# Optimization experiments

Hardware: AMD Instinct MI355X
Metric: run time of the kernel (lower is better)

## Reference

```python
import jax, jax.numpy as jnp
import numpy as np

B, D, H, Z, E = 2048, 1024, 1024, 256, 64


def setup_inputs() -> dict:
    key = jax.random.key(0)
    ks = jax.random.split(key, 16)
    s = lambda k, shape, std=0.02: jax.random.normal(k, shape, dtype=jnp.float32) * std
    return {
        "x": jax.random.normal(ks[0], (B, D), dtype=jnp.float32),
        "h0": jax.random.normal(ks[1], (B, H), dtype=jnp.float32),
        "c0": jax.random.normal(ks[2], (B, H), dtype=jnp.float32),
        "hhat0": jax.random.normal(ks[3], (B, Z), dtype=jnp.float32),
        "chat0": jax.random.normal(ks[4], (B, Z), dtype=jnp.float32),
        "hweight": s(ks[5], (Z + H + D, 4 * Z)),
        "hbias": jnp.zeros((4 * Z,), jnp.float32),
        "zweight_h": s(ks[6], (Z, 4 * E), 0.01),
        "zweight_x": s(ks[7], (Z, 4 * E), 0.01),
        "zweight_b": s(ks[8], (Z, 4 * E), 0.01),
        "zbias_h": jnp.ones((4 * E,), jnp.float32),
        "zbias_x": jnp.ones((4 * E,), jnp.float32),
        # stacked in gate order (i, g, f, o), matching the torch cat order
        "dweight_h": jnp.full((4, E, H), 0.1 / E, jnp.float32),
        "dweight_x": jnp.full((4, E, H), 0.1 / E, jnp.float32),
        "dweight_b": s(ks[9], (4, E, H), 0.01),
        "weight": s(ks[10], (H + D, 4 * H)),
        "bias": jnp.zeros((4 * H,), jnp.float32),
    }


def reference(x, h0, c0, hhat0, chat0, hweight, hbias,
              zweight_h, zweight_x, zweight_b, zbias_h, zbias_x,
              dweight_h, dweight_x, dweight_b, weight, bias):
    # ---- hyper LSTM cell ----
    hcat = jnp.concatenate([hhat0, h0, x], axis=1)                 # [B, Z+H+D]
    hg = hcat @ hweight + hbias                                    # [B, 4Z]
    i_h, g_h, f_h, o_h = jnp.split(hg, 4, axis=1)
    chat1 = jax.nn.sigmoid(f_h) * chat0 + jax.nn.sigmoid(i_h) * jnp.tanh(g_h)
    hhat1 = jax.nn.sigmoid(o_h) * jnp.tanh(chat1)                  # [B, Z]

    # ---- embeddings z (gate order i, g, f, o) ----
    z_h = (hhat1 @ zweight_h + zbias_h).reshape(-1, 4, E)          # [B,4,E]
    z_x = (hhat1 @ zweight_x + zbias_x).reshape(-1, 4, E)
    z_b = (hhat1 @ zweight_b).reshape(-1, 4, E)

    # ---- per-gate modulation vectors d_y* : [B,4,H] -> [B,4H] ----
    d_yh = jnp.einsum('bge,geh->bgh', z_h, dweight_h).reshape(-1, 4 * H)
    d_yx = jnp.einsum('bge,geh->bgh', z_x, dweight_x).reshape(-1, 4 * H)
    d_yb = jnp.einsum('bge,geh->bgh', z_b, dweight_b).reshape(-1, 4 * H)

    # ---- main LSTM with hypernetwork modulation ----
    gates = jnp.concatenate([h0, x], axis=1) @ weight              # [B, 4H]
    gates = gates * d_yh * d_yx + d_yb + bias
    i_g, g_g, f_g, o_g = jnp.split(gates, 4, axis=1)
    c1 = jax.nn.sigmoid(f_g) * c0 + jax.nn.sigmoid(i_g) * jnp.tanh(g_g)
    h1 = jax.nn.sigmoid(o_g) * jnp.tanh(c1)
    return (h1, c1, hhat1, chat1)
```

## Files before the change

### kernel.cpp

```cpp
#include <hip/hip_runtime.h>
#include <hip/hip_bf16.h>
#include <math.h>


typedef __attribute__((ext_vector_type(8))) short bf16x8;
typedef __attribute__((ext_vector_type(4))) float f32x4;
typedef unsigned short u16;

__device__ __forceinline__ u16 f2b(float f) {
  union { float f; unsigned u; } v; v.f = f;
  unsigned r = v.u + 0x7fffu + ((v.u >> 16) & 1u);
  return (u16)(r >> 16);
}
__device__ __forceinline__ float b2f(u16 b) {
  union { unsigned u; float f; } v; v.u = ((unsigned)b) << 16; return v.f;
}
__device__ __forceinline__ float sigm(float x) {
  return __builtin_amdgcn_rcpf(1.f + __expf(-x));
}
__device__ __forceinline__ float ftanh(float x) {
  float xc = fminf(fmaxf(x, -15.f), 15.f);
  float t = __expf(2.f * xc);
  return (t - 1.f) * __builtin_amdgcn_rcpf(t + 1.f);
}
__device__ __forceinline__ float sel4(float a, float b, float c, float d, int k) {
  return (k & 2) ? ((k & 1) ? d : c) : ((k & 1) ? b : a);
}

#define GLL16(gsrc, ldst)                                                      \
  __builtin_amdgcn_global_load_lds(                                            \
      (const __attribute__((address_space(1))) void*)(gsrc),                   \
      (__attribute__((address_space(3))) void*)(ldst), 16, 0, 0)

__global__ void k_prep(const float* __restrict__ hhat0, const float* __restrict__ h0,
                       const float* __restrict__ x, const float* __restrict__ weight,
                       const float* __restrict__ hweight,
                       const float* __restrict__ zw_h, const float* __restrict__ zw_x,
                       const float* __restrict__ zw_b, const float* __restrict__ dw_h,
                       const float* __restrict__ dw_x, const float* __restrict__ dw_b,
                       u16* __restrict__ hcatb, u16* __restrict__ bt,
                       u16* __restrict__ zwT, u16* __restrict__ dwT) {
  __shared__ float tile[32][66];
  int bid = blockIdx.x;
  const int t = threadIdx.x;
  if (bid < 4608) {
    int i = bid * 256 + t;
    int b = i / 576, c4 = i % 576;
    const float* src;
    if (c4 < 64)       src = hhat0 + (long)b * 256 + c4 * 4;
    else if (c4 < 320) src = h0 + (long)b * 1024 + (c4 - 64) * 4;
    else               src = x + (long)b * 1024 + (c4 - 320) * 4;
    float4 v = *(const float4*)src;
    ushort4 o = {f2b(v.x), f2b(v.y), f2b(v.z), f2b(v.w)};
    *(ushort4*)&hcatb[(long)b * 2304 + c4 * 4] = o;
    return;
  }
  bid -= 4608;
  if (bid < 5760) {
    const int n0 = (bid % 160) * 32, k0 = (bid / 160) * 64;
    if (n0 < 4096 && k0 < 256) return;
    const int isH = (n0 >= 4096);
    const float* src; int C, sc0, sr0;
    if (isH) { src = hweight; C = 1024; sc0 = n0 - 4096; sr0 = k0; }
    else     { src = weight;  C = 4096; sc0 = n0;        sr0 = k0 - 256; }
    #pragma unroll
    for (int p = 0; p < 8; ++p) {
      int c = t & 31, r = (t >> 5) + 8 * p;
      tile[c][r] = src[(long)(sr0 + r) * C + sc0 + c];
    }
    __syncthreads();
    #pragma unroll
    for (int p = 0; p < 2; ++p) {
      int kc = t & 15, cl = (t >> 4) + 16 * p;
      int orow;
      if (isH) { int u = sc0 + cl; orow = 4096 + ((u & 255) << 2) + (u >> 8); }
      else     orow = n0 + cl;
      ushort4 o = {f2b(tile[cl][4 * kc]), f2b(tile[cl][4 * kc + 1]),
                   f2b(tile[cl][4 * kc + 2]), f2b(tile[cl][4 * kc + 3])};
      *(ushort4*)&bt[(long)orow * 2304 + k0 + 4 * kc] = o;
    }
    return;
  }
  bid -= 5760;
  const int zi = bid >> 5, bx = bid & 31;
  const float* src; u16* dst; int R, C;
  if (zi < 3) {
    src = (zi == 0) ? zw_h : (zi == 1) ? zw_x : zw_b;
    dst = zwT + (long)zi * 65536; R = 256; C = 256;
  } else {
    int s = zi - 3, tt = s >> 2, g = s & 3;
    src = ((tt == 0) ? dw_h : (tt == 1) ? dw_x : dw_b) + (long)g * 65536;
    dst = dwT + (long)s * 65536; R = 64; C = 1024;
  }
  const int nct = C / 32;
  const int c0 = (bx % nct) * 32, r0 = (bx / nct) * 64;
  #pragma unroll
  for (int p = 0; p < 8; ++p) {
    int c = t & 31, r = (t >> 5) + 8 * p;
    tile[c][r] = src[(long)(r0 + r) * C + c0 + c];
  }
  __syncthreads();
  #pragma unroll
  for (int p = 0; p < 2; ++p) {
    int kc = t & 15, cl = (t >> 4) + 16 * p;
    ushort4 o = {f2b(tile[cl][4 * kc]), f2b(tile[cl][4 * kc + 1]),
                 f2b(tile[cl][4 * kc + 2]), f2b(tile[cl][4 * kc + 3])};
    *(ushort4*)&dst[(long)(c0 + cl) * R + r0 + 4 * kc] = o;
  }
}

__global__ __launch_bounds__(512, 4)
void k_gemm_main(const u16* __restrict__ A, const u16* __restrict__ Bt,
                 const float* __restrict__ hbias, const float* __restrict__ chat0,
                 u16* __restrict__ grawb, float* __restrict__ chat1,
                 float* __restrict__ hhat1, u16* __restrict__ hhat1b) {
  constexpr int K = 2304, BK = 64;
  __shared__ __align__(16) u16 sA[128 * BK];
  __shared__ __align__(16) u16 sB[128 * BK];
  const int m0 = blockIdx.y * 128, n0 = blockIdx.x * 128;
  const int kstart = (n0 < 4096) ? 256 : 0;
  const int tid = threadIdx.x, wave = tid >> 6, lane = tid & 63;
  const int quad = lane >> 4, lrow = lane & 15;
  const int wm = (wave >> 2) * 64, wn = (wave & 3) * 32;

  const int la = tid * 16;
  const int rowa = la >> 7, qa = (((la >> 4) & 7) - rowa) & 7;
  const int lb = 8192 + tid * 16;
  const int rowb = lb >> 7, qb = (((lb >> 4) & 7) - rowb) & 7;
  const long aoff0 = ((long)(m0 + rowa) * K + qa * 8) * 2;
  const long aoff1 = ((long)(m0 + rowb) * K + qb * 8) * 2;
  const long boff0 = ((long)(n0 + rowa) * K + qa * 8) * 2;
  const long boff1 = ((long)(n0 + rowb) * K + qb * 8) * 2;

  const f32x4 vz = {0.f, 0.f, 0.f, 0.f};
  f32x4 acc[4][2];
  #pragma unroll
  for (int i = 0; i < 4; ++i)
    #pragma unroll
    for (int j = 0; j < 2; ++j) acc[i][j] = vz;

  for (int k0 = kstart; k0 < K; k0 += BK) {
    GLL16((const char*)A + aoff0 + (long)k0 * 2, (char*)sA + wave * 1024);
    GLL16((const char*)A + aoff1 + (long)k0 * 2, (char*)sA + 8192 + wave * 1024);
    GLL16((const char*)Bt + boff0 + (long)k0 * 2, (char*)sB + wave * 1024);
    GLL16((const char*)Bt + boff1 + (long)k0 * 2, (char*)sB + 8192 + wave * 1024);
    __syncthreads();

    bf16x8 af[4][2], bf[2][2];
    #pragma unroll
    for (int i = 0; i < 4; ++i) {
      int row = wm + i * 16 + lrow;
      const char* base = (const char*)sA + row * 128;
      af[i][0] = *(const bf16x8*)(base + (((quad + row) & 7) << 4));
      af[i][1] = *(const bf16x8*)(base + (((4 + quad + row) & 7) << 4));
    }
    #pragma unroll
    for (int j = 0; j < 2; ++j) {
      int row = wn + j * 16 + lrow;
      const char* base = (const char*)sB + row * 128;
      bf[j][0] = *(const bf16x8*)(base + (((quad + row) & 7) << 4));
      bf[j][1] = *(const bf16x8*)(base + (((4 + quad + row) & 7) << 4));
    }
    #pragma unroll
    for (int kk = 0; kk < 2; ++kk)
      #pragma unroll
      for (int i = 0; i < 4; ++i)
        #pragma unroll
        for (int j = 0; j < 2; ++j)
          acc[i][j] = __builtin_amdgcn_mfma_f32_16x16x32_bf16(af[i][kk], bf[j][kk], acc[i][j], 0, 0, 0);
    __syncthreads();
  }

  if (n0 < 4096) {
    #pragma unroll
    for (int i = 0; i < 4; ++i)
      #pragma unroll
      for (int j = 0; j < 2; ++j)
        #pragma unroll
        for (int r = 0; r < 4; ++r) {
          int row = m0 + wm + i * 16 + quad * 4 + r;
          int col = n0 + wn + j * 16 + lrow;
          grawb[(long)row * 4096 + col] = f2b(acc[i][j][r]);
        }
  } else {
    const int ubase = (n0 - 4096) + wn;
    const int q3 = lane & 3;
    #pragma unroll
    for (int i = 0; i < 4; ++i) {
      #pragma unroll
      for (int j = 0; j < 2; ++j) {
        int u = ubase + j * 16 + lrow;
        int g = u & 3, z = u >> 2;
        float hb = hbias[g * 256 + z];
        float v0 = acc[i][j][0] + hb, v1 = acc[i][j][1] + hb;
        float v2 = acc[i][j][2] + hb, v3 = acc[i][j][3] + hb;
        float s0 = sel4(v0, v1, v2, v3, q3);
        float s1 = __shfl_xor(sel4(v0, v1, v2, v3, q3 ^ 1), 1);
        float s2 = __shfl_xor(sel4(v0, v1, v2, v3, q3 ^ 2), 2);
        float s3 = __shfl_xor(sel4(v0, v1, v2, v3, q3 ^ 3), 3);
        float vi = sel4(s0, s1, s2, s3, q3);
        float vg = sel4(s0, s1, s2, s3, q3 ^ 1);
        float vf = sel4(s0, s1, s2, s3, q3 ^ 2);
        float vo = sel4(s0, s1, s2, s3, q3 ^ 3);
        int row = m0 + wm + i * 16 + quad * 4 + q3;
        float cc = sigm(vf) * chat0[(long)row * 256 + z] + sigm(vi) * ftanh(vg);
        float hh = sigm(vo) * ftanh(cc);
        chat1[(long)row * 256 + z] = cc;
        hhat1[(long)row * 256 + z] = hh;
        hhat1b[(long)row * 256 + z] = f2b(hh);
      }
    }
  }
}

__global__ __launch_bounds__(256, 2)
void k_gemm_z(const u16* __restrict__ A, const u16* __restrict__ Bt,
              const float* __restrict__ zbh, const float* __restrict__ zbx,
              u16* __restrict__ zbout) {
  constexpr int K = 256, BK = 32;
  __shared__ __align__(16) u16 sA[64 * BK];
  __shared__ __align__(16) u16 sB[128 * BK];
  const int m0 = blockIdx.y * 64, n0 = blockIdx.x * 128;
  const int tid = threadIdx.x, wave = tid >> 6, lane = tid & 63;
  const int quad = lane >> 4, lrow = lane & 15;
  const int wm = (wave >> 1) * 32, wn = (wave & 1) * 64;

  const int sl = tid * 16;
  const int arow = sl >> 6;
  const int aq = (((sl & 63) >> 4) - (arow >> 1)) & 3;
  const long aoff = ((long)(m0 + arow) * K) * 2 + aq * 16;

  const f32x4 vz = {0.f, 0.f, 0.f, 0.f};
  f32x4 acc[2][4];
  #pragma unroll
  for (int i = 0; i < 2; ++i)
    #pragma unroll
    for (int j = 0; j < 4; ++j) acc[i][j] = vz;

  for (int k0 = 0; k0 < K; k0 += BK) {
    GLL16((const char*)A + aoff + (long)k0 * 2, (char*)sA + wave * 1024);
    #pragma unroll
    for (int c = 0; c < 2; ++c) {
      int l = c * 4096 + sl;
      int row = l >> 6;
      int q = (((l & 63) >> 4) - (row >> 1)) & 3;
      const char* g = (const char*)Bt + ((long)(n0 + row) * K + k0) * 2 + q * 16;
      GLL16(g, (char*)sB + c * 4096 + wave * 1024);
    }
    __syncthreads();
    bf16x8 af[2], bf[4];
    #pragma unroll
    for (int i = 0; i < 2; ++i) {
      int row = wm + i * 16 + lrow;
      af[i] = *(const bf16x8*)((const char*)sA + row * 64 + (((quad + (row >> 1)) & 3) << 4));
    }
    #pragma unroll
    for (int j = 0; j < 4; ++j) {
      int row = wn + j * 16 + lrow;
      bf[j] = *(const bf16x8*)((const char*)sB + row * 64 + (((quad + (row >> 1)) & 3) << 4));
    }
    #pragma unroll
    for (int i = 0; i < 2; ++i)
      #pragma unroll
      for (int j = 0; j < 4; ++j)
        acc[i][j] = __builtin_amdgcn_mfma_f32_16x16x32_bf16(af[i], bf[j], acc[i][j], 0, 0, 0);
    __syncthreads();
  }
  #pragma unroll
  for (int i = 0; i < 2; ++i) {
    #pragma unroll
    for (int j = 0; j < 4; ++j) {
      #pragma unroll
      for (int r = 0; r < 4; ++r) {
        int row = m0 + wm + i * 16 + quad * 4 + r;
        int col = n0 + wn + j * 16 + lrow;
        float v = acc[i][j][r] + ((col < 256) ? zbh[col] : (col < 512) ? zbx[col - 256] : 0.f);
        zbout[(long)row * 768 + col] = f2b(v);
      }
    }
  }
}

__global__ __launch_bounds__(256, 2)
void k_dmod_lstm(const u16* __restrict__ z, const u16* __restrict__ dwT,
                 const u16* __restrict__ grawb, const float* __restrict__ bias,
                 const float* __restrict__ c0, float* __restrict__ h1,
                 float* __restrict__ c1) {
  __shared__ __align__(16) u16 sZ[64 * 192];
  __shared__ __align__(16) u16 sW[3 * 64 * 64];
  __shared__ __align__(16) u16 sG[2][64 * 64];
  const int m0 = blockIdx.y * 64;
  const int hc0 = blockIdx.x * 64;
  const int tid = threadIdx.x, wave = tid >> 6, lane = tid & 63;
  const int quad = lane >> 4, lrow = lane & 15;
  const int wm = (wave >> 1) * 32, wn = (wave & 1) * 32;
  const f32x4 vz4 = {0.f, 0.f, 0.f, 0.f};

  f32x4 pcar[2][2];
  f32x4 ccar[2][2];

  auto stage = [&](int g) {
    #pragma unroll
    for (int c = 0; c < 6; ++c) {
      int l = c * 4096 + tid * 16;
      int ci = l >> 4, row = ci / 24, p = ci - row * 24;
      int q = p + 72 - row; q -= (q / 24) * 24;
      int tt = q >> 3, e16 = q & 7;
      const char* gz = (const char*)z + (long)(m0 + row) * 1536 + tt * 512 + g * 128 + e16 * 16;
      GLL16(gz, (char*)sZ + c * 4096 + wave * 1024);
      int t2 = l >> 13, rw = (l & 8191) >> 7, p2 = (l >> 4) & 7;
      int q2 = (p2 - rw) & 7;
      const char* gw = (const char*)dwT + (long)((t2 * 4 + g) * 1024 + hc0 + rw) * 128 + q2 * 16;
      GLL16(gw, (char*)sW + c * 4096 + wave * 1024);
    }
    #pragma unroll
    for (int c = 0; c < 2; ++c) {
      int l = c * 4096 + tid * 16;
      int row = l >> 7, off = l & 127;
      const char* gg = (const char*)grawb + ((long)(m0 + row) * 4096 + g * 1024 + hc0) * 2 + off;
      GLL16(gg, (char*)sG[g & 1] + c * 4096 + wave * 1024);
    }
  };

  stage(0);
  #pragma unroll
  for (int g = 0; g < 4; ++g) {
    __syncthreads();
    bf16x8 za2[2][3][2], wb2[2][3][2];
    #pragma unroll
    for (int kk = 0; kk < 2; ++kk) {
      #pragma unroll
      for (int t = 0; t < 3; ++t) {
        #pragma unroll
        for (int i = 0; i < 2; ++i) {
          int row = wm + i * 16 + lrow;
          int q0 = t * 8 + kk * 4 + quad;
          int ph = q0 + row; ph -= (ph / 24) * 24;
          za2[kk][t][i] = *(const bf16x8*)((const char*)sZ + row * 384 + ph * 16);
        }
        #pragma unroll
        for (int j = 0; j < 2; ++j) {
          int row = wn + j * 16 + lrow;
          int ph = ((kk * 4 + quad) + row) & 7;
          wb2[kk][t][j] = *(const bf16x8*)((const char*)sW + t * 8192 + row * 128 + ph * 16);
        }
      }
    }
    __syncthreads();
    if (g < 3) stage(g + 1);
    f32x4 aH[2][2], aX[2][2], aB[2][2];
    #pragma unroll
    for (int i = 0; i < 2; ++i)
      #pragma unroll
      for (int j = 0; j < 2; ++j) { aH[i][j] = vz4; aX[i][j] = vz4; aB[i][j] = vz4; }
    #pragma unroll
    for (int kk = 0; kk < 2; ++kk)
      #pragma unroll
      for (int i = 0; i < 2; ++i)
        #pragma unroll
        for (int j = 0; j < 2; ++j) {
          aH[i][j] = __builtin_amdgcn_mfma_f32_16x16x32_bf16(za2[kk][0][i], wb2[kk][0][j], aH[i][j], 0, 0, 0);
          aX[i][j] = __builtin_amdgcn_mfma_f32_16x16x32_bf16(za2[kk][1][i], wb2[kk][1][j], aX[i][j], 0, 0, 0);
          aB[i][j] = __builtin_amdgcn_mfma_f32_16x16x32_bf16(za2[kk][2][i], wb2[kk][2][j], aB[i][j], 0, 0, 0);
        }
    const u16* sGc = sG[g & 1];
    #pragma unroll
    for (int i = 0; i < 2; ++i) {
      #pragma unroll
      for (int j = 0; j < 2; ++j) {
        #pragma unroll
        for (int r = 0; r < 4; ++r) {
          int rowl = wm + i * 16 + quad * 4 + r;
          int col = wn + j * 16 + lrow;
          int row = m0 + rowl;
          float gr = b2f(sGc[rowl * 64 + col]);
          float v = gr * aH[i][j][r] * aX[i][j][r] + aB[i][j][r] + bias[g * 1024 + hc0 + col];
          long idx = (long)row * 1024 + hc0 + col;
          if (g == 0) pcar[i][j][r] = sigm(v);
          else if (g == 1) pcar[i][j][r] *= ftanh(v);
          else if (g == 2) {
            float cc = sigm(v) * c0[idx] + pcar[i][j][r];
            ccar[i][j][r] = cc;
            c1[idx] = cc;
          } else {
            h1[idx] = sigm(v) * ftanh(ccar[i][j][r]);
          }
        }
      }
    }
  }
}


extern "C" void kernel_launch(void* const* d_in, const int* in_sizes, int n_in,
                              void* d_out, int out_size, void* d_ws, size_t ws_size,
                              hipStream_t stream) {
  const float* x      = (const float*)d_in[0];
  const float* h0     = (const float*)d_in[1];
  const float* c0     = (const float*)d_in[2];
  const float* hhat0  = (const float*)d_in[3];
  const float* chat0  = (const float*)d_in[4];
  const float* hweight= (const float*)d_in[5];
  const float* hbias  = (const float*)d_in[6];
  const float* zw_h   = (const float*)d_in[7];
  const float* zw_x   = (const float*)d_in[8];
  const float* zw_b   = (const float*)d_in[9];
  const float* zb_h   = (const float*)d_in[10];
  const float* zb_x   = (const float*)d_in[11];
  const float* dw_h   = (const float*)d_in[12];
  const float* dw_x   = (const float*)d_in[13];
  const float* dw_b   = (const float*)d_in[14];
  const float* weight = (const float*)d_in[15];
  const float* bias   = (const float*)d_in[16];
  float* out = (float*)d_out;

  char* w = (char*)d_ws;
  auto take = [&](size_t bytes) { char* p = w; w += (bytes + 255) & ~(size_t)255; return p; };
  u16*   hcatb  = (u16*)take(2048ull * 2304 * 2);
  u16*   btc    = (u16*)take(5120ull * 2304 * 2);
  u16*   zwT    = (u16*)take(768ull * 256 * 2);
  u16*   dwT    = (u16*)take(12ull * 1024 * 64 * 2);
  u16*   grawb  = (u16*)take(2048ull * 4096 * 2);
  u16*   hhat1b = (u16*)take(2048ull * 256 * 2);
  u16*   zb16   = (u16*)take(2048ull * 768 * 2);

  float* h1_o    = out;
  float* c1_o    = out + 2048 * 1024;
  float* hhat1_o = out + 2 * 2048 * 1024;
  float* chat1_o = out + 2 * 2048 * 1024 + 2048 * 256;

  k_prep<<<4608 + 5760 + 480, 256, 0, stream>>>(
      hhat0, h0, x, weight, hweight, zw_h, zw_x, zw_b, dw_h, dw_x, dw_b,
      hcatb, btc, zwT, dwT);

  k_gemm_main<<<dim3(40, 16), 512, 0, stream>>>(hcatb, btc, hbias, chat0,
                                                grawb, chat1_o, hhat1_o, hhat1b);

  k_gemm_z<<<dim3(6, 32), 256, 0, stream>>>(hhat1b, zwT, zb_h, zb_x, zb16);

  k_dmod_lstm<<<dim3(16, 32), 256, 0, stream>>>(zb16, dwT, grawb, bias, c0, h1_o, c1_o);
}
```

Before: 217.8 us.

## Double-buffer LDS tiles in main GEMM to overlap global loads with MFMA

The main GEMM's shared-memory tiles become two buffers, and the next K-tile's global-to-LDS loads are issued before computing on the current one. A partial vmcnt wait plus barriers separates the stages, so global load latency can overlap MFMA work. LDS use per block doubles to 64KB, which may cut how many blocks fit per CU under launch_bounds(512,4).

```diff
diff --git a/kernel.cpp b/kernel.cpp
--- a/kernel.cpp
+++ b/kernel.cpp
@@ -115,8 +115,8 @@
                  u16* __restrict__ grawb, float* __restrict__ chat1,
                  float* __restrict__ hhat1, u16* __restrict__ hhat1b) {
   constexpr int K = 2304, BK = 64;
-  __shared__ __align__(16) u16 sA[128 * BK];
-  __shared__ __align__(16) u16 sB[128 * BK];
+  __shared__ __align__(16) u16 sA[2][128 * BK];
+  __shared__ __align__(16) u16 sB[2][128 * BK];
   const int m0 = blockIdx.y * 128, n0 = blockIdx.x * 128;
   const int kstart = (n0 < 4096) ? 256 : 0;
   const int tid = threadIdx.x, wave = tid >> 6, lane = tid & 63;
@@ -139,25 +139,29 @@
     #pragma unroll
     for (int j = 0; j < 2; ++j) acc[i][j] = vz;
 
-  for (int k0 = kstart; k0 < K; k0 += BK) {
-    GLL16((const char*)A + aoff0 + (long)k0 * 2, (char*)sA + wave * 1024);
-    GLL16((const char*)A + aoff1 + (long)k0 * 2, (char*)sA + 8192 + wave * 1024);
-    GLL16((const char*)Bt + boff0 + (long)k0 * 2, (char*)sB + wave * 1024);
-    GLL16((const char*)Bt + boff1 + (long)k0 * 2, (char*)sB + 8192 + wave * 1024);
-    __syncthreads();
-
+  auto stage = [&](int d, int k0) {
+    const long kb = (long)k0 * 2;
+    GLL16((const char*)A + aoff0 + kb, (char*)sA[d] + wave * 1024);
+    GLL16((const char*)A + aoff1 + kb, (char*)sA[d] + 8192 + wave * 1024);
+    GLL16((const char*)Bt + boff0 + kb, (char*)sB[d] + wave * 1024);
+    GLL16((const char*)Bt + boff1 + kb, (char*)sB[d] + 8192 + wave * 1024);
+  };
+
+  auto compute = [&](int d) {
     bf16x8 af[4][2], bf[2][2];
+    const char* pA = (const char*)sA[d];
+    const char* pB = (const char*)sB[d];
     #pragma unroll
     for (int i = 0; i < 4; ++i) {
       int row = wm + i * 16 + lrow;
-      const char* base = (const char*)sA + row * 128;
+      const char* base = pA + row * 128;
       af[i][0] = *(const bf16x8*)(base + (((quad + row) & 7) << 4));
       af[i][1] = *(const bf16x8*)(base + (((4 + quad + row) & 7) << 4));
     }
     #pragma unroll
     for (int j = 0; j < 2; ++j) {
       int row = wn + j * 16 + lrow;
-      const char* base = (const char*)sB + row * 128;
+      const char* base = pB + row * 128;
       bf[j][0] = *(const bf16x8*)(base + (((quad + row) & 7) << 4));
       bf[j][1] = *(const bf16x8*)(base + (((4 + quad + row) & 7) << 4));
     }
@@ -168,8 +172,23 @@
         #pragma unroll
         for (int j = 0; j < 2; ++j)
           acc[i][j] = __builtin_amdgcn_mfma_f32_16x16x32_bf16(af[i][kk], bf[j][kk], acc[i][j], 0, 0, 0);
-    __syncthreads();
-  }
+  };
+
+  const int nt = (K - kstart) >> 6;
+  stage(0, kstart);
+  for (int t = 0; t < nt - 1; ++t) {
+    stage((t + 1) & 1, kstart + (t + 1) * BK);
+    asm volatile("s_waitcnt vmcnt(4)" ::: "memory");
+    __builtin_amdgcn_sched_barrier(0);
+    __builtin_amdgcn_s_barrier();
+    __builtin_amdgcn_sched_barrier(0);
+    compute(t & 1);
+    __builtin_amdgcn_s_barrier();
+  }
+  asm volatile("s_waitcnt vmcnt(0)" ::: "memory");
+  __builtin_amdgcn_sched_barrier(0);
+  __builtin_amdgcn_s_barrier();
+  compute((nt - 1) & 1);
 
   if (n0 < 4096) {
     #pragma unroll
```

After: 225.4 us. 1.03x slower.
